# Performance work log

Hardware: AMD Instinct MI355X
Metric: run time of the kernel (lower is better)

Reference implementation:

```python
import jax, jax.numpy as jnp
import numpy as np

N = 50000        # nodes
E = 800000       # edges (pre self-loops)
H = 1            # heads
D = 64           # out_channels (incl. Lorentz time coord)
IN = 128         # in_channels
C = 1.0          # curvature c (Lorentz k)
EPS = 1e-6
NEG = 0.2        # leaky_relu negative slope


def segment_softmax(logits, seg, n):
    # numerically stable softmax over edges grouped by destination node
    m = jax.ops.segment_max(logits, seg, num_segments=n)
    m = jnp.where(jnp.isfinite(m), m, 0.0)
    e = jnp.exp(logits - m[seg])
    s = jax.ops.segment_sum(e, seg, num_segments=n)
    return e / (s[seg] + 1e-16)


def setup_inputs() -> dict:
    key = jax.random.key(0)
    k1, k2, k3, k4, k5 = jax.random.split(key, 5)
    x = jax.random.normal(k1, (N, IN), jnp.float32)
    fan = IN + H * (D - 1)
    W = jax.random.uniform(k2, (IN, H * (D - 1)), jnp.float32, -1.0, 1.0) * (6.0 / fan) ** 0.5
    b = jnp.zeros((H * (D - 1),), jnp.float32)
    att = jax.random.uniform(k3, (1, H, 2 * D), jnp.float32, -1.0, 1.0) * (6.0 / (H + 2 * D)) ** 0.5
    # random edges with no self loops (module removes them then re-adds canonical loops)
    src = jax.random.randint(k4, (E,), 0, N, jnp.int32)
    off = jax.random.randint(k5, (E,), 1, N, jnp.int32)
    dst = (src + off) % N
    edge_index = jnp.stack([src, dst], axis=0)
    return {"x": x, "W": W, "b": b, "att": att, "edge_index": edge_index}


def reference(x, W, b, att, edge_index):
    sqrt_c = C ** 0.5
    # add self loops
    loops = jnp.arange(N, dtype=edge_index.dtype)
    ei = jnp.concatenate([edge_index, jnp.stack([loops, loops])], axis=1)
    i, j = ei[0], ei[1]

    # hy_linear (plain Linear on Lorentz branch), then project to hyperboloid
    xs = (x @ W + b).reshape(N, H, D - 1)                       # space coords
    t = jnp.sqrt(jnp.sum(xs * xs, -1, keepdims=True) + C)       # time coord
    ox = jnp.concatenate([t, xs], -1)                           # (N,H,D) on manifold

    # Lorentz logmap0: d0 * (0, xs/||xs||), d0 = sqrt(c)*arccosh(x0/sqrt(c))
    nrm = jnp.sqrt(jnp.sum(xs * xs, -1, keepdims=True) + 1e-15)
    d0 = sqrt_c * jnp.arccosh(jnp.maximum(t / sqrt_c, 1.0 + EPS))
    log_x = jnp.concatenate([jnp.zeros_like(t), d0 * xs / nrm], -1)  # (N,H,D)

    x_i, x_j = log_x[i], log_x[j]        # (E2,H,D) edge gathers
    ox_i, ox_j = ox[i], ox[j]

    # attention logits
    alpha = jnp.sum(jnp.concatenate([x_i, x_j], -1) * att, -1)  # (E2,H)

    # distance-aware weighting: sqdist = c * arccosh(-<x,y>_L / c)^2
    inner = -ox_i[..., 0] * ox_j[..., 0] + jnp.sum(ox_i[..., 1:] * ox_j[..., 1:], -1)
    sqd = C * jnp.arccosh(jnp.maximum(-inner / C, 1.0 + EPS)) ** 2
    alpha = alpha * segment_softmax(sqd, i, N)

    alpha = jnp.where(alpha >= 0, alpha, NEG * alpha)           # leaky_relu
    alpha = segment_softmax(alpha, i, N)                        # (E2,H)

    out = jax.ops.segment_sum(alpha[..., None] * x_j, i, num_segments=N)  # (N,H,D)

    # proj_tan0 -> act -> proj_tan0
    out = out.at[..., 0].set(0.0)
    out = jax.nn.relu(out)
    out = out.at[..., 0].set(0.0)

    # expmap0 then projx
    usp = out[..., 1:]
    un = jnp.sqrt(jnp.sum(usp * usp, -1, keepdims=True) + 1e-15)
    sp = sqrt_c * jnp.sinh(un / sqrt_c) * usp / un
    time = jnp.sqrt(jnp.sum(sp * sp, -1, keepdims=True) + C)    # projx recomputes time
    y = jnp.concatenate([time, sp], -1)
    return y.reshape(N, H * D)
```

## Files before the change

### kernel.cpp

```cpp
#include <hip/hip_runtime.h>
#include <math.h>

#define NN 50000
#define EE 800000
#define ETOT 850000
#define INF 128
#define DD 64
#define NB_NODE 1024
#define NB_EDGE ((ETOT + 255) / 256)

__device__ __forceinline__ float wsum64(float v) {
#pragma unroll
    for (int m = 1; m < 64; m <<= 1) v += __shfl_xor(v, m, 64);
    return v;
}
__device__ __forceinline__ float wmax64(float v) {
#pragma unroll
    for (int m = 1; m < 64; m <<= 1) v = fmaxf(v, __shfl_xor(v, m, 64));
    return v;
}
__device__ __forceinline__ float rl(float v, int k) {
    return __int_as_float(__builtin_amdgcn_readlane(__float_as_int(v), k));
}

__device__ __forceinline__ float mink_inner(const float* __restrict__ ox,
                                            int j, float xnv) {
    const float4* ojp = (const float4*)(ox + (size_t)j * DD);
    float4 oj[16];
#pragma unroll
    for (int q = 0; q < 16; ++q) oj[q] = ojp[q];
    float p0 = 0.f, p1 = 0.f, p2 = 0.f, p3 = 0.f;
#pragma unroll
    for (int q = 0; q < 16; ++q) {
        p0 = fmaf(rl(xnv, 4 * q + 0), oj[q].x, p0);
        p1 = fmaf(rl(xnv, 4 * q + 1), oj[q].y, p1);
        p2 = fmaf(rl(xnv, 4 * q + 2), oj[q].z, p2);
        p3 = fmaf(rl(xnv, 4 * q + 3), oj[q].w, p3);
    }
    return (p0 + p1 + p2 + p3) - 2.f * rl(xnv, 0) * oj[0].x;
}

__global__ __launch_bounds__(256) void k_node_deg(
    const float* __restrict__ x, const float* __restrict__ W,
    const float* __restrict__ b, const float* __restrict__ att,
    const int* __restrict__ ei0,
    float* __restrict__ ox, float* __restrict__ ai, float2* __restrict__ snd,
    int* __restrict__ deg, int* __restrict__ posbuf)
{
    if (blockIdx.x >= NB_NODE) {
        int e = (blockIdx.x - NB_NODE) * 256 + threadIdx.x;
        if (e < ETOT) {
            int i = (e < EE) ? ei0[e] : (e - EE);
            posbuf[e] = atomicAdd(&deg[i], 1);
        }
        return;
    }

    const int lane = threadIdx.x & 63;
    const int wid  = threadIdx.x >> 6;
    const int wgid = blockIdx.x * 4 + wid;
    const int nw   = NB_NODE * 4;

    const int col = (lane == 0) ? 0 : lane - 1;
    float wreg[INF];
#pragma unroll
    for (int k = 0; k < INF; ++k) wreg[k] = W[k * (DD - 1) + col];
    const float bcol = b[col];
    const float atti = att[lane];
    const float attj = att[DD + lane];

    float nxv0 = x[(size_t)wgid * INF + lane];
    float nxv1 = x[(size_t)wgid * INF + 64 + lane];

    for (int n = wgid; n < NN; n += nw) {
        float xv0 = nxv0, xv1 = nxv1;
        int np = n + nw;
        if (np < NN) {
            nxv0 = x[(size_t)np * INF + lane];
            nxv1 = x[(size_t)np * INF + 64 + lane];
        }
        float acc0 = 0.f, acc1 = 0.f;
#pragma unroll
        for (int k = 0; k < 64; k += 2) {
            acc0 = fmaf(rl(xv0, k),     wreg[k],     acc0);
            acc1 = fmaf(rl(xv0, k + 1), wreg[k + 1], acc1);
        }
#pragma unroll
        for (int k = 0; k < 64; k += 2) {
            acc0 = fmaf(rl(xv1, k),     wreg[64 + k],     acc0);
            acc1 = fmaf(rl(xv1, k + 1), wreg[64 + k + 1], acc1);
        }
        float xs = (lane == 0) ? 0.f : (acc0 + acc1 + bcol);

        float ss  = wsum64(xs * xs);
        float t   = sqrtf(ss + 1.0f);
        float nrm = sqrtf(ss + 1e-15f);
        float d0  = acoshf(fmaxf(t, 1.0f + 1e-6f));
        float scl = d0 / nrm;

        ox[(size_t)n * DD + lane] = (lane == 0) ? t : xs;
        float lxv = (lane == 0) ? 0.f : scl * xs;

        float aiv = wsum64(lxv * atti);
        float ajv = wsum64(lxv * attj);
        if (lane == 0) { ai[n] = aiv; snd[n] = make_float2(ajv, scl); }
    }
}

__global__ __launch_bounds__(256) void k_scan1(
    const int* __restrict__ deg, int* __restrict__ rowptr, int* __restrict__ bsum)
{
    __shared__ int tmp[256];
    int tid = threadIdx.x;
    int gid = blockIdx.x * 256 + tid;
    int v = (gid < NN) ? deg[gid] : 0;
    tmp[tid] = v; __syncthreads();
    for (int off = 1; off < 256; off <<= 1) {
        int t = (tid >= off) ? tmp[tid - off] : 0;
        __syncthreads();
        tmp[tid] += t;
        __syncthreads();
    }
    if (gid < NN) rowptr[gid + 1] = tmp[tid];
    if (tid == 255) bsum[blockIdx.x] = tmp[255];
}

__global__ __launch_bounds__(256) void k_scan2(int* __restrict__ bsum, int nb)
{
    __shared__ int tmp[256];
    int tid = threadIdx.x;
    int v = (tid < nb) ? bsum[tid] : 0;
    tmp[tid] = v; __syncthreads();
    for (int off = 1; off < 256; off <<= 1) {
        int t = (tid >= off) ? tmp[tid - off] : 0;
        __syncthreads();
        tmp[tid] += t;
        __syncthreads();
    }
    if (tid < nb) bsum[tid] = tmp[tid];
}

__global__ __launch_bounds__(256) void k_scan3(
    int* __restrict__ rowptr, const int* __restrict__ bsum)
{
    int gid = blockIdx.x * 256 + threadIdx.x;
    if (gid < NN) {
        int add = (blockIdx.x > 0) ? bsum[blockIdx.x - 1] : 0;
        rowptr[gid + 1] += add;
    }
    if (gid == 0) rowptr[0] = 0;
}

__global__ __launch_bounds__(256) void k_place(
    const int* __restrict__ ei0, const int* __restrict__ ei1,
    const int* __restrict__ rowptr, const int* __restrict__ posbuf,
    int* __restrict__ colA)
{
    int e = blockIdx.x * blockDim.x + threadIdx.x;
    if (e >= ETOT) return;
    int i, j;
    if (e < EE) { i = ei0[e]; j = ei1[e]; }
    else        { i = e - EE; j = i; }
    colA[rowptr[i] + posbuf[e]] = j;
}

__global__ __launch_bounds__(256) void k_fused(
    const int* __restrict__ rowptr, const int* __restrict__ colA,
    const float* __restrict__ ox, const float* __restrict__ ai,
    const float2* __restrict__ snd,
    float* __restrict__ ebuf, float* __restrict__ y)
{
    const int lane = threadIdx.x & 63;
    const int wid  = threadIdx.x >> 6;
    const int n = blockIdx.x * 4 + wid;
    if (n >= NN) return;

    const int base = rowptr[n];
    const int deg  = rowptr[n + 1] - base;
    const float aii = ai[n];
    const float xnv = ox[(size_t)n * DD + lane];

    float acc = 0.f;

    if (deg <= 64) {
        const bool act = lane < deg;
        const int  ecl = min(lane, deg - 1);
        const int  jreg = colA[base + ecl];
        const float2 sv = snd[jreg];

        float inner = mink_inner(ox, jreg, xnv);
        float arg = fmaxf(-inner, 1.0f + 1e-6f);
        float dd0 = acoshf(arg);
        float sq  = act ? dd0 * dd0 : -3e38f;

        float m1 = wmax64(sq);
        float e1 = act ? expf(sq - m1) : 0.f;
        float s1 = wsum64(e1) + 1e-16f;
        float al = (aii + sv.x) * e1 / s1;
        al = (al >= 0.f) ? al : 0.2f * al;
        float m2 = wmax64(act ? al : -3e38f);
        float p2 = act ? expf(al - m2) : 0.f;
        float s2 = wsum64(p2);
        float w2 = p2 / (s2 + 1e-16f) * sv.y;

        int k = 0;
        for (; k + 8 <= deg; k += 8) {
            float w0 = __shfl(w2, k + 0, 64), w1 = __shfl(w2, k + 1, 64);
            float w2b = __shfl(w2, k + 2, 64), w3 = __shfl(w2, k + 3, 64);
            float w4 = __shfl(w2, k + 4, 64), w5 = __shfl(w2, k + 5, 64);
            float w6 = __shfl(w2, k + 6, 64), w7 = __shfl(w2, k + 7, 64);
            int j0 = __shfl(jreg, k + 0, 64), j1 = __shfl(jreg, k + 1, 64);
            int j2 = __shfl(jreg, k + 2, 64), j3 = __shfl(jreg, k + 3, 64);
            int j4 = __shfl(jreg, k + 4, 64), j5 = __shfl(jreg, k + 5, 64);
            int j6 = __shfl(jreg, k + 6, 64), j7 = __shfl(jreg, k + 7, 64);
            float v0 = ox[(size_t)j0 * DD + lane], v1 = ox[(size_t)j1 * DD + lane];
            float v2 = ox[(size_t)j2 * DD + lane], v3 = ox[(size_t)j3 * DD + lane];
            float v4 = ox[(size_t)j4 * DD + lane], v5 = ox[(size_t)j5 * DD + lane];
            float v6 = ox[(size_t)j6 * DD + lane], v7 = ox[(size_t)j7 * DD + lane];
            acc = fmaf(w0, v0, acc);  acc = fmaf(w1, v1, acc);
            acc = fmaf(w2b, v2, acc); acc = fmaf(w3, v3, acc);
            acc = fmaf(w4, v4, acc);  acc = fmaf(w5, v5, acc);
            acc = fmaf(w6, v6, acc);  acc = fmaf(w7, v7, acc);
        }
        for (; k < deg; ++k) {
            float w = __shfl(w2, k, 64);
            int   j = __shfl(jreg, k, 64);
            acc = fmaf(w, ox[(size_t)j * DD + lane], acc);
        }
    } else {
        float m1 = -3e38f;
        for (int k0 = 0; k0 < deg; k0 += 64) {
            int e = k0 + lane;
            bool act = e < deg;
            int ec = min(e, deg - 1);
            int j = colA[base + ec];
            float inner = mink_inner(ox, j, xnv);
            float arg = fmaxf(-inner, 1.0f + 1e-6f);
            float dd0 = acoshf(arg);
            float sq = dd0 * dd0;
            if (act) ebuf[base + e] = sq;
            m1 = fmaxf(m1, act ? sq : -3e38f);
        }
        m1 = wmax64(m1);

        float s1p = 0.f;
        for (int k0 = 0; k0 < deg; k0 += 64) {
            int e = k0 + lane;
            if (e < deg) s1p += expf(ebuf[base + e] - m1);
        }
        float s1 = wsum64(s1p) + 1e-16f;

        float m2l = -3e38f;
        for (int k0 = 0; k0 < deg; k0 += 64) {
            int e = k0 + lane;
            if (e < deg) {
                int j = colA[base + e];
                float2 sv = snd[j];
                float al = (aii + sv.x) * expf(ebuf[base + e] - m1) / s1;
                al = (al >= 0.f) ? al : 0.2f * al;
                ebuf[base + e] = al;
                m2l = fmaxf(m2l, al);
            }
        }
        float m2 = wmax64(m2l);

        float s2p = 0.f;
        for (int k0 = 0; k0 < deg; k0 += 64) {
            int e = k0 + lane;
            if (e < deg) s2p += expf(ebuf[base + e] - m2);
        }
        float s2 = wsum64(s2p) + 1e-16f;

        for (int k = 0; k < deg; ++k) {
            int j = colA[base + k];
            float2 sv = snd[j];
            float w = expf(ebuf[base + k] - m2) / s2 * sv.y;
            acc = fmaf(w, ox[(size_t)j * DD + lane], acc);
        }
    }

    float usp = (lane == 0) ? 0.f : fmaxf(acc, 0.f);
    float ss = wsum64(usp * usp);
    float un = sqrtf(ss + 1e-15f);
    float sc = sinhf(un) / un;
    float sp = sc * usp;
    float time = sqrtf(sc * sc * ss + 1.0f);
    y[(size_t)n * DD + lane] = (lane == 0) ? time : sp;
}

extern "C" void kernel_launch(void* const* d_in, const int* in_sizes, int n_in,
                              void* d_out, int out_size, void* d_ws, size_t ws_size,
                              hipStream_t stream) {
    const float* x   = (const float*)d_in[0];
    const float* W   = (const float*)d_in[1];
    const float* b   = (const float*)d_in[2];
    const float* att = (const float*)d_in[3];
    const int*   ei  = (const int*)d_in[4];
    const int* ei0 = ei;
    const int* ei1 = ei + EE;
    float* out = (float*)d_out;

    float*  ws  = (float*)d_ws;
    float*  ox  = ws;
    float*  ai  = ox + (size_t)NN * DD;
    float2* snd = (float2*)(ai + NN);
    int*    deg    = (int*)(snd + NN);
    int*    rowptr = deg + NN;
    int*    bsum   = rowptr + NN + 1;
    int*    colA   = bsum + 256;
    int*    posbuf = colA + ETOT;
    float*  ebuf   = (float*)posbuf;

    const int nb1 = (NN + 255) / 256;

    hipMemsetAsync(deg, 0, sizeof(int) * NN, stream);

    k_node_deg<<<NB_NODE + NB_EDGE, 256, 0, stream>>>(
        x, W, b, att, ei0, ox, ai, snd, deg, posbuf);

    k_scan1<<<nb1, 256, 0, stream>>>(deg, rowptr, bsum);
    k_scan2<<<1, 256, 0, stream>>>(bsum, nb1);
    k_scan3<<<nb1, 256, 0, stream>>>(rowptr, bsum);
    k_place<<<(ETOT + 255) / 256, 256, 0, stream>>>(ei0, ei1, rowptr, posbuf, colA);

    k_fused<<<(NN + 3) / 4, 256, 0, stream>>>(rowptr, colA, ox, ai, snd, ebuf, out);
}
```

Baseline: 158.1 us.

## Replace three-pass scan with atomic wave allocation and add transposed-reduce fast path

Replaces the three-kernel prefix scan with a single kernel in which each wave scans its degrees and reserves a contiguous range through one atomicAdd. Rows no longer sit in node order, so k_fused reads the degree array directly. For nodes of degree up to 16 or 32, each lane now computes partial Minkowski products from coalesced row loads, and these are combined with a butterfly transpose-reduce instead of each lane loading a whole 64-float row. This is meant to cut launch count and the uncoalesced per-lane row gathers, at the cost of more shuffles and a non-deterministic CSR order.

```diff
diff --git a/kernel.cpp b/kernel.cpp
--- a/kernel.cpp
+++ b/kernel.cpp
@@ -19,25 +19,27 @@
     for (int m = 1; m < 64; m <<= 1) v = fmaxf(v, __shfl_xor(v, m, 64));
     return v;
 }
-__device__ __forceinline__ float rl(float v, int k) {
+__device__ __forceinline__ float rlf(float v, int k) {
     return __int_as_float(__builtin_amdgcn_readlane(__float_as_int(v), k));
 }
-
-__device__ __forceinline__ float mink_inner(const float* __restrict__ ox,
+__device__ __forceinline__ int rli(int v, int k) {
+    return __builtin_amdgcn_readlane(v, k);
+}
+
+__device__ __forceinline__ float mink_light(const float* __restrict__ ox,
                                             int j, float xnv) {
-    const float4* ojp = (const float4*)(ox + (size_t)j * DD);
-    float4 oj[16];
-#pragma unroll
-    for (int q = 0; q < 16; ++q) oj[q] = ojp[q];
-    float p0 = 0.f, p1 = 0.f, p2 = 0.f, p3 = 0.f;
-#pragma unroll
+    const float4* ojp = (const float4*)(ox + (size_t)(unsigned)j * DD);
+    float pa = 0.f, y0 = 0.f;
+#pragma unroll 4
     for (int q = 0; q < 16; ++q) {
-        p0 = fmaf(rl(xnv, 4 * q + 0), oj[q].x, p0);
-        p1 = fmaf(rl(xnv, 4 * q + 1), oj[q].y, p1);
-        p2 = fmaf(rl(xnv, 4 * q + 2), oj[q].z, p2);
-        p3 = fmaf(rl(xnv, 4 * q + 3), oj[q].w, p3);
-    }
-    return (p0 + p1 + p2 + p3) - 2.f * rl(xnv, 0) * oj[0].x;
+        float4 o = ojp[q];
+        if (q == 0) y0 = o.x;
+        pa = fmaf(rlf(xnv, 4 * q + 0), o.x, pa);
+        pa = fmaf(rlf(xnv, 4 * q + 1), o.y, pa);
+        pa = fmaf(rlf(xnv, 4 * q + 2), o.z, pa);
+        pa = fmaf(rlf(xnv, 4 * q + 3), o.w, pa);
+    }
+    return pa - 2.f * rlf(xnv, 0) * y0;
 }
 
 __global__ __launch_bounds__(256) void k_node_deg(
@@ -82,13 +84,13 @@
         float acc0 = 0.f, acc1 = 0.f;
 #pragma unroll
         for (int k = 0; k < 64; k += 2) {
-            acc0 = fmaf(rl(xv0, k),     wreg[k],     acc0);
-            acc1 = fmaf(rl(xv0, k + 1), wreg[k + 1], acc1);
+            acc0 = fmaf(rlf(xv0, k),     wreg[k],     acc0);
+            acc1 = fmaf(rlf(xv0, k + 1), wreg[k + 1], acc1);
         }
 #pragma unroll
         for (int k = 0; k < 64; k += 2) {
-            acc0 = fmaf(rl(xv1, k),     wreg[64 + k],     acc0);
-            acc1 = fmaf(rl(xv1, k + 1), wreg[64 + k + 1], acc1);
+            acc0 = fmaf(rlf(xv1, k),     wreg[64 + k],     acc0);
+            acc1 = fmaf(rlf(xv1, k + 1), wreg[64 + k + 1], acc1);
         }
         float xs = (lane == 0) ? 0.f : (acc0 + acc1 + bcol);
 
@@ -107,48 +109,23 @@
     }
 }
 
-__global__ __launch_bounds__(256) void k_scan1(
-    const int* __restrict__ deg, int* __restrict__ rowptr, int* __restrict__ bsum)
-{
-    __shared__ int tmp[256];
-    int tid = threadIdx.x;
-    int gid = blockIdx.x * 256 + tid;
-    int v = (gid < NN) ? deg[gid] : 0;
-    tmp[tid] = v; __syncthreads();
-    for (int off = 1; off < 256; off <<= 1) {
-        int t = (tid >= off) ? tmp[tid - off] : 0;
-        __syncthreads();
-        tmp[tid] += t;
-        __syncthreads();
-    }
-    if (gid < NN) rowptr[gid + 1] = tmp[tid];
-    if (tid == 255) bsum[blockIdx.x] = tmp[255];
-}
-
-__global__ __launch_bounds__(256) void k_scan2(int* __restrict__ bsum, int nb)
-{
-    __shared__ int tmp[256];
-    int tid = threadIdx.x;
-    int v = (tid < nb) ? bsum[tid] : 0;
-    tmp[tid] = v; __syncthreads();
-    for (int off = 1; off < 256; off <<= 1) {
-        int t = (tid >= off) ? tmp[tid - off] : 0;
-        __syncthreads();
-        tmp[tid] += t;
-        __syncthreads();
-    }
-    if (tid < nb) bsum[tid] = tmp[tid];
-}
-
-__global__ __launch_bounds__(256) void k_scan3(
-    int* __restrict__ rowptr, const int* __restrict__ bsum)
-{
-    int gid = blockIdx.x * 256 + threadIdx.x;
-    if (gid < NN) {
-        int add = (blockIdx.x > 0) ? bsum[blockIdx.x - 1] : 0;
-        rowptr[gid + 1] += add;
-    }
-    if (gid == 0) rowptr[0] = 0;
+__global__ __launch_bounds__(256) void k_alloc(
+    const int* __restrict__ deg, int* __restrict__ rowptr, int* __restrict__ gcount)
+{
+    int gid  = blockIdx.x * 256 + threadIdx.x;
+    int lane = threadIdx.x & 63;
+    int d = (gid < NN) ? deg[gid] : 0;
+    int sc = d;
+#pragma unroll
+    for (int m = 1; m < 64; m <<= 1) {
+        int t = __shfl_up(sc, m, 64);
+        if (lane >= m) sc += t;
+    }
+    int tot = __shfl(sc, 63, 64);
+    int bw = 0;
+    if (lane == 0) bw = atomicAdd(gcount, tot);
+    bw = __shfl(bw, 0, 64);
+    if (gid < NN) rowptr[gid] = bw + sc - d;
 }
 
 __global__ __launch_bounds__(256) void k_place(
@@ -164,8 +141,73 @@
     colA[rowptr[i] + posbuf[e]] = j;
 }
 
+template<int K>
+__device__ __forceinline__ float fast_node(
+    const int* __restrict__ colA, const float* __restrict__ ox,
+    const float2* __restrict__ snd, int base, int deg,
+    float aii, float oxs, int lane)
+{
+    const int  ecl  = min(lane, deg - 1);
+    const int  jreg = colA[base + ecl];
+    const float2 sv = snd[jreg];
+
+    float p[K];
+#pragma unroll
+    for (int k = 0; k < K; ++k) {
+        if (k < deg) {
+            int jk = rli(jreg, k);
+            p[k] = oxs * ox[(size_t)(unsigned)jk * DD + lane];
+        } else {
+            p[k] = 0.f;
+        }
+    }
+
+    constexpr int LOGK = (K == 16) ? 4 : 5;
+#pragma unroll
+    for (int b = 0; b < LOGK; ++b) {
+        const int s = (lane >> b) & 1;
+#pragma unroll
+        for (int t = 0; t < (K >> (b + 1)); ++t) {
+            float a0 = p[2 * t], a1 = p[2 * t + 1];
+            float keep = s ? a1 : a0;
+            float send = s ? a0 : a1;
+            float recv = __shfl_xor(send, 1 << b, 64);
+            p[t] = keep + recv;
+        }
+    }
+    float inner = p[0];
+#pragma unroll
+    for (int m = K; m < 64; m <<= 1) inner += __shfl_xor(inner, m, 64);
+
+    const bool act = lane < deg;
+    float arg = fmaxf(-inner, 1.0f + 1e-6f);
+    float dd0 = acoshf(arg);
+    float sq  = act ? dd0 * dd0 : -3e38f;
+    float m1 = wmax64(sq);
+    float e1 = act ? expf(sq - m1) : 0.f;
+    float s1 = wsum64(e1) + 1e-16f;
+    float al = (aii + sv.x) * e1 / s1;
+    al = (al >= 0.f) ? al : 0.2f * al;
+    float m2 = wmax64(act ? al : -3e38f);
+    float p2 = act ? expf(al - m2) : 0.f;
+    float s2 = wsum64(p2);
+    float w2 = p2 / (s2 + 1e-16f) * sv.y;
+
+    float acc = 0.f;
+#pragma unroll
+    for (int k = 0; k < K; ++k) {
+        if (k < deg) {
+            float wk = rlf(w2, k);
+            int   jk = rli(jreg, k);
+            acc = fmaf(wk, ox[(size_t)(unsigned)jk * DD + lane], acc);
+        }
+    }
+    return acc;
+}
+
 __global__ __launch_bounds__(256) void k_fused(
-    const int* __restrict__ rowptr, const int* __restrict__ colA,
+    const int* __restrict__ rowptr, const int* __restrict__ degA,
+    const int* __restrict__ colA,
     const float* __restrict__ ox, const float* __restrict__ ai,
     const float2* __restrict__ snd,
     float* __restrict__ ebuf, float* __restrict__ y)
@@ -176,57 +218,16 @@
     if (n >= NN) return;
 
     const int base = rowptr[n];
-    const int deg  = rowptr[n + 1] - base;
+    const int deg  = degA[n];
     const float aii = ai[n];
     const float xnv = ox[(size_t)n * DD + lane];
+    const float oxs = (lane == 0) ? -xnv : xnv;
 
     float acc = 0.f;
-
-    if (deg <= 64) {
-        const bool act = lane < deg;
-        const int  ecl = min(lane, deg - 1);
-        const int  jreg = colA[base + ecl];
-        const float2 sv = snd[jreg];
-
-        float inner = mink_inner(ox, jreg, xnv);
-        float arg = fmaxf(-inner, 1.0f + 1e-6f);
-        float dd0 = acoshf(arg);
-        float sq  = act ? dd0 * dd0 : -3e38f;
-
-        float m1 = wmax64(sq);
-        float e1 = act ? expf(sq - m1) : 0.f;
-        float s1 = wsum64(e1) + 1e-16f;
-        float al = (aii + sv.x) * e1 / s1;
-        al = (al >= 0.f) ? al : 0.2f * al;
-        float m2 = wmax64(act ? al : -3e38f);
-        float p2 = act ? expf(al - m2) : 0.f;
-        float s2 = wsum64(p2);
-        float w2 = p2 / (s2 + 1e-16f) * sv.y;
-
-        int k = 0;
-        for (; k + 8 <= deg; k += 8) {
-            float w0 = __shfl(w2, k + 0, 64), w1 = __shfl(w2, k + 1, 64);
-            float w2b = __shfl(w2, k + 2, 64), w3 = __shfl(w2, k + 3, 64);
-            float w4 = __shfl(w2, k + 4, 64), w5 = __shfl(w2, k + 5, 64);
-            float w6 = __shfl(w2, k + 6, 64), w7 = __shfl(w2, k + 7, 64);
-            int j0 = __shfl(jreg, k + 0, 64), j1 = __shfl(jreg, k + 1, 64);
-            int j2 = __shfl(jreg, k + 2, 64), j3 = __shfl(jreg, k + 3, 64);
-            int j4 = __shfl(jreg, k + 4, 64), j5 = __shfl(jreg, k + 5, 64);
-            int j6 = __shfl(jreg, k + 6, 64), j7 = __shfl(jreg, k + 7, 64);
-            float v0 = ox[(size_t)j0 * DD + lane], v1 = ox[(size_t)j1 * DD + lane];
-            float v2 = ox[(size_t)j2 * DD + lane], v3 = ox[(size_t)j3 * DD + lane];
-            float v4 = ox[(size_t)j4 * DD + lane], v5 = ox[(size_t)j5 * DD + lane];
-            float v6 = ox[(size_t)j6 * DD + lane], v7 = ox[(size_t)j7 * DD + lane];
-            acc = fmaf(w0, v0, acc);  acc = fmaf(w1, v1, acc);
-            acc = fmaf(w2b, v2, acc); acc = fmaf(w3, v3, acc);
-            acc = fmaf(w4, v4, acc);  acc = fmaf(w5, v5, acc);
-            acc = fmaf(w6, v6, acc);  acc = fmaf(w7, v7, acc);
-        }
-        for (; k < deg; ++k) {
-            float w = __shfl(w2, k, 64);
-            int   j = __shfl(jreg, k, 64);
-            acc = fmaf(w, ox[(size_t)j * DD + lane], acc);
-        }
+    if (deg <= 16) {
+        acc = fast_node<16>(colA, ox, snd, base, deg, aii, oxs, lane);
+    } else if (deg <= 32) {
+        acc = fast_node<32>(colA, ox, snd, base, deg, aii, oxs, lane);
     } else {
         float m1 = -3e38f;
         for (int k0 = 0; k0 < deg; k0 += 64) {
@@ -234,7 +235,7 @@
             bool act = e < deg;
             int ec = min(e, deg - 1);
             int j = colA[base + ec];
-            float inner = mink_inner(ox, j, xnv);
+            float inner = mink_light(ox, j, xnv);
             float arg = fmaxf(-inner, 1.0f + 1e-6f);
             float dd0 = acoshf(arg);
             float sq = dd0 * dd0;
@@ -305,23 +306,19 @@
     float*  ai  = ox + (size_t)NN * DD;
     float2* snd = (float2*)(ai + NN);
     int*    deg    = (int*)(snd + NN);
-    int*    rowptr = deg + NN;
-    int*    bsum   = rowptr + NN + 1;
-    int*    colA   = bsum + 256;
+    int*    gcount = deg + NN;
+    int*    rowptr = gcount + 1;
+    int*    colA   = rowptr + NN;
     int*    posbuf = colA + ETOT;
     float*  ebuf   = (float*)posbuf;
 
-    const int nb1 = (NN + 255) / 256;
-
-    hipMemsetAsync(deg, 0, sizeof(int) * NN, stream);
+    hipMemsetAsync(deg, 0, sizeof(int) * (NN + 1), stream);
 
     k_node_deg<<<NB_NODE + NB_EDGE, 256, 0, stream>>>(
         x, W, b, att, ei0, ox, ai, snd, deg, posbuf);
 
-    k_scan1<<<nb1, 256, 0, stream>>>(deg, rowptr, bsum);
-    k_scan2<<<1, 256, 0, stream>>>(bsum, nb1);
-    k_scan3<<<nb1, 256, 0, stream>>>(rowptr, bsum);
+    k_alloc<<<(NN + 255) / 256, 256, 0, stream>>>(deg, rowptr, gcount);
     k_place<<<(ETOT + 255) / 256, 256, 0, stream>>>(ei0, ei1, rowptr, posbuf, colA);
 
-    k_fused<<<(NN + 3) / 4, 256, 0, stream>>>(rowptr, colA, ox, ai, snd, ebuf, out);
-}
+    k_fused<<<(NN + 3) / 4, 256, 0, stream>>>(rowptr, deg, colA, ox, ai, snd, ebuf, out);
+}
```

Result: slower. 176.4 us (+11.5%).
